# Performance work log

Measured on AMD Instinct MI355X. Metric: run time of the kernel, lower is better.

## Reference

```python
import jax, jax.numpy as jnp
import numpy as np

EPS = 1e-12
SIMILARITY = 'l2'


def setup_inputs() -> dict:
    key = jax.random.key(0)
    k1, k2, k3, k4 = jax.random.split(key, 4)
    N, M, D = 8192, 8192, 256
    x = jax.random.normal(k1, (N, D), dtype=jnp.float32)
    x_n = jax.random.normal(k2, (M, D), dtype=jnp.float32)
    W = jax.random.normal(k3, (D, 2), dtype=jnp.float32) / np.sqrt(D)
    b = jax.random.normal(k4, (2,), dtype=jnp.float32)
    return {"x": x, "x_n": x_n, "W": W, "b": b}


def _sim_matrix(x, x_n, similarity):
    if similarity == 'l2':
        x2 = jnp.sum(x * x, axis=1, keepdims=True)          # [N,1]
        xn2 = jnp.sum(x_n * x_n, axis=1, keepdims=True).T    # [1,M]
        d2 = jnp.maximum(x2 + xn2 - 2.0 * (x @ x_n.T), 0.0)
        return -jnp.sqrt(d2)
    elif similarity == 'l1':
        return -jnp.sum(jnp.abs(x[:, None, :] - x_n[None, :, :]), axis=-1)
    elif similarity == 'dot':
        return (x @ x_n.T) / x.shape[1]
    elif similarity == 'cos':
        xn_ = x / jnp.linalg.norm(x, axis=1, keepdims=True)
        xnn = x_n / jnp.linalg.norm(x_n, axis=1, keepdims=True)
        return xn_ @ xnn.T
    raise ValueError(similarity)


def reference(x, x_n, W, b) -> jnp.ndarray:
    # soft-KNN params from a small linear head
    params = jax.nn.sigmoid(x @ W + b)                      # [N,2]
    k = jnp.clip(params[:, 0:1], EPS, 1.0 - EPS)            # [N,1]
    t = jnp.clip(params[:, 1:2], EPS, 1.0 - EPS)            # [N,1]

    sim = _sim_matrix(x, x_n, SIMILARITY)                   # [N,M]
    sim_min = jnp.min(sim, axis=1, keepdims=True)
    sim_max = jnp.max(sim, axis=1, keepdims=True)
    sim = (sim - sim_min) / (sim_max - sim_min)             # row min-max normalize
    sim = jnp.maximum(sim, EPS)

    shift = t / (1.0 - t) * (k - sim) * jnp.log(sim / k)
    return sim + jnp.where(sim <= k, shift, 0.0)
```

## Files before the change

### kernel.cpp

```cpp
#include <hip/hip_runtime.h>
#include <hip/hip_bf16.h>
#include <hip/hip_fp16.h>
#include <cstdint>

#define N_ROWS 8192
#define M_ROWS 8192
#define DDIM   256
#define EPSF   1e-12f
#define NT     4

typedef unsigned short u16;
typedef __attribute__((ext_vector_type(8))) short short8;
typedef __attribute__((ext_vector_type(4))) float floatx4;

__device__ inline u16 f2h(float v) {
    return __builtin_bit_cast(u16, (_Float16)v);
}
__device__ inline void split_bf16(float v, u16& h, u16& lo) {
    __hip_bfloat16 hb = __float2bfloat16(v);
    float hf = __bfloat162float(hb);
    __hip_bfloat16 lb = __float2bfloat16(v - hf);
    h  = __builtin_bit_cast(u16, hb);
    lo = __builtin_bit_cast(u16, lb);
}

__global__ __launch_bounds__(256) void prep_x(
    const float* __restrict__ x, const float* __restrict__ W, const float* __restrict__ b,
    u16* __restrict__ xh, float* __restrict__ x2, float* __restrict__ karr,
    float* __restrict__ Carr, float* __restrict__ logkarr, u16* __restrict__ bfprobe)
{
    const int l = threadIdx.x & 63;
    const int w = threadIdx.x >> 6;
    const int row = blockIdx.x * 4 + w;

    const float4 xv = *(const float4*)(x + (size_t)row * DDIM + l * 4);
    const float4 wa = *(const float4*)(W + l * 8);
    const float4 wb = *(const float4*)(W + l * 8 + 4);

    float s2 = xv.x * xv.x + xv.y * xv.y + xv.z * xv.z + xv.w * xv.w;
    float s0 = xv.x * wa.x + xv.y * wa.z + xv.z * wb.x + xv.w * wb.z;
    float s1 = xv.x * wa.y + xv.y * wa.w + xv.z * wb.y + xv.w * wb.w;

    *(ushort4*)(xh + (size_t)row * DDIM + l * 4) =
        make_ushort4(f2h(xv.x), f2h(xv.y), f2h(xv.z), f2h(xv.w));

    if (row == 0 && l == 0 && w == 0) {
        u16 hh, ll; split_bf16(xv.x, hh, ll);
        bfprobe[0] = hh; bfprobe[1] = ll;
    }

    #pragma unroll
    for (int off = 32; off; off >>= 1) {
        s2 += __shfl_xor(s2, off);
        s0 += __shfl_xor(s0, off);
        s1 += __shfl_xor(s1, off);
    }
    if (l == 0) {
        float a0 = s0 + b[0];
        float a1 = s1 + b[1];
        float k = 1.0f / (1.0f + __expf(-a0));
        float t = 1.0f / (1.0f + __expf(-a1));
        k = fminf(fmaxf(k, EPSF), 1.0f - EPSF);
        t = fminf(fmaxf(t, EPSF), 1.0f - EPSF);
        x2[row] = s2;
        karr[row] = k;
        Carr[row] = t / (1.0f - t);
        logkarr[row] = logf(k);
    }
}

__global__ __launch_bounds__(256) void prep_xn(
    const float* __restrict__ xn, u16* __restrict__ xnh, float* __restrict__ xn2)
{
    const int l = threadIdx.x & 63;
    const int w = threadIdx.x >> 6;
    const int row = blockIdx.x * 4 + w;

    const float4 xv = *(const float4*)(xn + (size_t)row * DDIM + l * 4);
    float s2 = xv.x * xv.x + xv.y * xv.y + xv.z * xv.z + xv.w * xv.w;

    *(ushort4*)(xnh + (size_t)row * DDIM + l * 4) =
        make_ushort4(f2h(xv.x), f2h(xv.y), f2h(xv.z), f2h(xv.w));

    #pragma unroll
    for (int off = 32; off; off >>= 1) s2 += __shfl_xor(s2, off);
    if (l == 0) xn2[row] = s2;
}

__global__ __launch_bounds__(512, 2) void gemm_s(
    const u16* __restrict__ xh, const u16* __restrict__ xnh,
    const float* __restrict__ x2, const float* __restrict__ xn2,
    float* __restrict__ out)
{
    extern __shared__ char lds[];

    const int tid = threadIdx.x;
    const int l   = tid & 63;
    const int w   = tid >> 6;
    const int wm  = w >> 2;
    const int wn  = w & 3;

    const int wg    = blockIdx.x;
    const int xcd   = wg & 7;
    const int seq   = wg >> 3;
    const int rnd   = seq >> 5;
    const int idx   = seq & 31;
    const int cell  = rnd * 8 + xcd;
    const int rg    = cell & 7;
    const int cg    = cell >> 3;
    const int bRow  = rg * 4 + (idx & 3);
    const int bCol  = cg * 8 + (idx >> 2);

    const int srow = tid >> 3;
    const int scol = (((tid & 7) ^ (srow & 7)) << 3);
    const int dcol = (tid & 7) * 16;
    const int rA1_0 = srow,               rA1_1 = srow + 128;
    const int rA2_0 = srow + 64,          rA2_1 = srow + 192;
    const int rB1_0 = srow + (srow & 32), rB1_1 = rB1_0 + 128;
    const int rB2_0 = rB1_0 + 32,         rB2_1 = rB1_0 + 160;
    const size_t aG = (size_t)bRow * 256;
    const size_t bG = (size_t)bCol * 256;

#define KOFF(T) ((T) * 64)
#define LDSA(T) (lds + ((T) & 1) * 65536)
#define LDSB(T) (lds + ((T) & 1) * 65536 + 32768)
#define SU(pan, gbase, ldsbase, r0, r1, ko) do {                                  \
    __builtin_amdgcn_global_load_lds(                                             \
        (const __attribute__((address_space(1))) void*)((pan) + ((gbase) + (r0)) * (size_t)DDIM + (ko) + scol), \
        (__attribute__((address_space(3))) void*)((ldsbase) + (r0) * 128 + dcol), 16, 0, 0); \
    __builtin_amdgcn_global_load_lds(                                             \
        (const __attribute__((address_space(1))) void*)((pan) + ((gbase) + (r1)) * (size_t)DDIM + (ko) + scol), \
        (__attribute__((address_space(3))) void*)((ldsbase) + (r1) * 128 + dcol), 16, 0, 0); \
} while (0)
#define SU_A1(T) SU(xh,  aG, LDSA(T), rA1_0, rA1_1, KOFF(T))
#define SU_A2(T) SU(xh,  aG, LDSA(T), rA2_0, rA2_1, KOFF(T))
#define SU_B1(T) SU(xnh, bG, LDSB(T), rB1_0, rB1_1, KOFF(T))
#define SU_B2(T) SU(xnh, bG, LDSB(T), rB2_0, rB2_1, KOFF(T))

    floatx4 acc[8][4];
    #pragma unroll
    for (int mi = 0; mi < 8; ++mi)
        #pragma unroll
        for (int ni = 0; ni < 4; ++ni)
            acc[mi][ni] = (floatx4){0.f, 0.f, 0.f, 0.f};

    const int laneRow = l & 15;
    const int laneKb  = (l >> 4) << 4;
    const int laneSwz = (l & 7) << 4;
    const int aRowB = (wm * 128 + laneRow) * 128;
    const int bRowB = (wn * 64  + laneRow) * 128;
    const int kb0 = laneKb ^ laneSwz;
    const int kb1 = (64 + laneKb) ^ laneSwz;

    SU_A1(0); SU_B1(0); SU_B2(0); SU_A2(0);
    SU_B1(1); SU_A1(1); SU_B2(1);

    short8 a[4][2], b01[2][2], b23[2][2];

    for (int t = 0; t < NT; ++t) {
        const char* pA = LDSA(t);
        const char* pB = LDSB(t);

        if (t < NT - 1) asm volatile("s_waitcnt vmcnt(6)" ::: "memory");
        else            asm volatile("s_waitcnt vmcnt(0)" ::: "memory");
        if (t + 1 < NT) SU_A2(t + 1);
        __builtin_amdgcn_s_barrier();
        #pragma unroll
        for (int mi = 0; mi < 4; ++mi) {
            a[mi][0] = *(const short8*)(pA + aRowB + mi * 2048 + kb0);
            a[mi][1] = *(const short8*)(pA + aRowB + mi * 2048 + kb1);
        }
        #pragma unroll
        for (int ni = 0; ni < 2; ++ni) {
            b01[ni][0] = *(const short8*)(pB + bRowB + ni * 2048 + kb0);
            b01[ni][1] = *(const short8*)(pB + bRowB + ni * 2048 + kb1);
        }
        asm volatile("s_waitcnt lgkmcnt(0)" ::: "memory");
        __builtin_amdgcn_sched_barrier(0);
        __builtin_amdgcn_s_setprio(1);
        #pragma unroll
        for (int mi = 0; mi < 4; ++mi)
            #pragma unroll
            for (int ni = 0; ni < 2; ++ni) {
                acc[mi][ni] = __builtin_amdgcn_mfma_f32_16x16x32_f16(a[mi][0], b01[ni][0], acc[mi][ni], 0, 0, 0);
                acc[mi][ni] = __builtin_amdgcn_mfma_f32_16x16x32_f16(a[mi][1], b01[ni][1], acc[mi][ni], 0, 0, 0);
            }
        __builtin_amdgcn_s_setprio(0);
        __builtin_amdgcn_sched_barrier(0);
        __builtin_amdgcn_s_barrier();

        if (t + 2 < NT) SU_B1(t + 2);
        #pragma unroll
        for (int ni = 0; ni < 2; ++ni) {
            b23[ni][0] = *(const short8*)(pB + bRowB + (2 + ni) * 2048 + kb0);
            b23[ni][1] = *(const short8*)(pB + bRowB + (2 + ni) * 2048 + kb1);
        }
        __builtin_amdgcn_s_barrier();
        asm volatile("s_waitcnt lgkmcnt(0)" ::: "memory");
        __builtin_amdgcn_sched_barrier(0);
        __builtin_amdgcn_s_setprio(1);
        #pragma unroll
        for (int mi = 0; mi < 4; ++mi)
            #pragma unroll
            for (int ni = 0; ni < 2; ++ni) {
                acc[mi][2 + ni] = __builtin_amdgcn_mfma_f32_16x16x32_f16(a[mi][0], b23[ni][0], acc[mi][2 + ni], 0, 0, 0);
                acc[mi][2 + ni] = __builtin_amdgcn_mfma_f32_16x16x32_f16(a[mi][1], b23[ni][1], acc[mi][2 + ni], 0, 0, 0);
            }
        __builtin_amdgcn_s_setprio(0);
        __builtin_amdgcn_sched_barrier(0);
        __builtin_amdgcn_s_barrier();

        if (t + 2 < NT) SU_A1(t + 2);
        #pragma unroll
        for (int mi = 0; mi < 4; ++mi) {
            a[mi][0] = *(const short8*)(pA + aRowB + (4 + mi) * 2048 + kb0);
            a[mi][1] = *(const short8*)(pA + aRowB + (4 + mi) * 2048 + kb1);
        }
        __builtin_amdgcn_s_barrier();
        asm volatile("s_waitcnt lgkmcnt(0)" ::: "memory");
        __builtin_amdgcn_sched_barrier(0);
        __builtin_amdgcn_s_setprio(1);
        #pragma unroll
        for (int mi = 0; mi < 4; ++mi)
            #pragma unroll
            for (int ni = 0; ni < 2; ++ni) {
                acc[4 + mi][ni] = __builtin_amdgcn_mfma_f32_16x16x32_f16(a[mi][0], b01[ni][0], acc[4 + mi][ni], 0, 0, 0);
                acc[4 + mi][ni] = __builtin_amdgcn_mfma_f32_16x16x32_f16(a[mi][1], b01[ni][1], acc[4 + mi][ni], 0, 0, 0);
            }
        __builtin_amdgcn_s_setprio(0);
        __builtin_amdgcn_sched_barrier(0);
        __builtin_amdgcn_s_barrier();

        if (t + 2 < NT) SU_B2(t + 2);
        __builtin_amdgcn_s_barrier();
        __builtin_amdgcn_s_setprio(1);
        #pragma unroll
        for (int mi = 0; mi < 4; ++mi)
            #pragma unroll
            for (int ni = 0; ni < 2; ++ni) {
                acc[4 + mi][2 + ni] = __builtin_amdgcn_mfma_f32_16x16x32_f16(a[mi][0], b23[ni][0], acc[4 + mi][2 + ni], 0, 0, 0);
                acc[4 + mi][2 + ni] = __builtin_amdgcn_mfma_f32_16x16x32_f16(a[mi][1], b23[ni][1], acc[4 + mi][2 + ni], 0, 0, 0);
            }
        __builtin_amdgcn_s_setprio(0);
        __builtin_amdgcn_sched_barrier(0);
        __builtin_amdgcn_s_barrier();
    }
#undef SU_A1
#undef SU_A2
#undef SU_B1
#undef SU_B2
#undef SU
#undef KOFF
#undef LDSA
#undef LDSB

    const int q  = l >> 4;
    const int cn = l & 15;
    const int rowBase = bRow * 256 + wm * 128;
    const int colBase = bCol * 256 + wn * 64;
    #pragma unroll
    for (int mi = 0; mi < 8; ++mi) {
        #pragma unroll
        for (int r = 0; r < 4; ++r) {
            const int i = rowBase + mi * 16 + q * 4 + r;
            const float x2i = x2[i];
            #pragma unroll
            for (int ni = 0; ni < 4; ++ni) {
                const int j = colBase + ni * 16 + cn;
                const float d2 = x2i + xn2[j] - 2.0f * acc[mi][ni][r];
                out[(size_t)i * M_ROWS + j] = -sqrtf(fmaxf(d2, 0.0f));
            }
        }
    }
}

__global__ __launch_bounds__(256) void transform_row(
    float* __restrict__ out, const float* __restrict__ x, const float* __restrict__ xn,
    const float* __restrict__ karr, const float* __restrict__ Carr,
    const float* __restrict__ logkarr)
{
    const int row = blockIdx.x;
    const int t = threadIdx.x;
    const int l = t & 63;
    const int w = t >> 6;

    __shared__ float wmin[4], wmax[4];
    __shared__ int cnt;
    __shared__ unsigned long long sMinBits;
    __shared__ int cidx[1024];
    __shared__ double cval[1024];

    const size_t rbase = (size_t)row * M_ROWS;
    float4 v[8];
    #pragma unroll
    for (int c = 0; c < 8; ++c)
        v[c] = *(const float4*)(out + rbase + c * 1024 + t * 4);

    float lmin = 1e30f, lmax = -1e30f;
    #pragma unroll
    for (int c = 0; c < 8; ++c) {
        lmin = fminf(lmin, fminf(fminf(v[c].x, v[c].y), fminf(v[c].z, v[c].w)));
        lmax = fmaxf(lmax, fmaxf(fmaxf(v[c].x, v[c].y), fmaxf(v[c].z, v[c].w)));
    }
    #pragma unroll
    for (int m = 1; m < 64; m <<= 1) {
        lmin = fminf(lmin, __shfl_xor(lmin, m));
        lmax = fmaxf(lmax, __shfl_xor(lmax, m));
    }
    if (l == 0) { wmin[w] = lmin; wmax[w] = lmax; }
    if (t == 0) { cnt = 0; sMinBits = 0ull; }
    __syncthreads();
    const float sminA = fminf(fminf(wmin[0], wmin[1]), fminf(wmin[2], wmin[3]));
    const float smaxA = fmaxf(fmaxf(wmax[0], wmax[1]), fmaxf(wmax[2], wmax[3]));
    const float thresh = sminA + 0.05f * (smaxA - sminA);

    int myPos[8], mySlot[8];
    int myCnt = 0;
    #pragma unroll
    for (int c = 0; c < 8; ++c) {
        const float* pv = (const float*)&v[c];
        #pragma unroll
        for (int u = 0; u < 4; ++u) {
            if (pv[u] <= thresh) {
                int pos = atomicAdd(&cnt, 1);
                if (pos < 1024 && myCnt < 8) {
                    cidx[pos] = c * 1024 + t * 4 + u;
                    myPos[myCnt] = pos;
                    mySlot[myCnt] = c * 4 + u;
                    myCnt++;
                }
            }
        }
    }
    __syncthreads();
    const int nc = min(cnt, 1024);

    const float4 xa = *(const float4*)(x + (size_t)row * DDIM + l * 4);
    const double dx0 = xa.x, dx1 = xa.y, dx2 = xa.z, dx3 = xa.w;
    double x2p = dx0 * dx0 + dx1 * dx1 + dx2 * dx2 + dx3 * dx3;
    #pragma unroll
    for (int m = 1; m < 64; m <<= 1) x2p += __shfl_xor(x2p, m);

    for (int c = w; c < nc; c += 4) {
        const int j = cidx[c];
        const float4 na = *(const float4*)(xn + (size_t)j * DDIM + l * 4);
        const double n0 = na.x, n1 = na.y, n2 = na.z, n3 = na.w;
        double dot = dx0 * n0 + dx1 * n1 + dx2 * n2 + dx3 * n3;
        double nn  = n0 * n0 + n1 * n1 + n2 * n2 + n3 * n3;
        #pragma unroll
        for (int m = 1; m < 64; m <<= 1) {
            dot += __shfl_xor(dot, m);
            nn  += __shfl_xor(nn, m);
        }
        if (l == 0) {
            double d2 = x2p + nn - 2.0 * dot;
            d2 = d2 > 0.0 ? d2 : 0.0;
            double se = -sqrt(d2);
            cval[c] = se;
            atomicMax(&sMinBits, (unsigned long long)__double_as_longlong(se));
        }
    }
    __syncthreads();

    const double sminD = __longlong_as_double((long long)sMinBits);
    const float k = karr[row], C = Carr[row], logk = logkarr[row];
    const float smin = (float)sminD;
    const double invD = 1.0 / ((double)smaxA - sminD);
    const float inv = (float)invD;

    float o[32];
    #pragma unroll
    for (int c = 0; c < 8; ++c) {
        const float* pv = (const float*)&v[c];
        #pragma unroll
        for (int u = 0; u < 4; ++u) {
            float sim = fmaxf((pv[u] - smin) * inv, EPSF);
            float r = sim;
            if (sim <= k) r += C * (k - sim) * (__logf(sim) - logk);
            o[c * 4 + u] = r;
        }
    }
    for (int q2 = 0; q2 < myCnt; ++q2) {
        double simd = (cval[myPos[q2]] - sminD) * invD;
        simd = simd > (double)EPSF ? simd : (double)EPSF;
        float sim = (float)simd;
        float r = sim;
        if (sim <= k) r += C * (k - sim) * (logf(sim) - logk);
        o[mySlot[q2]] = r;
    }
    #pragma unroll
    for (int c = 0; c < 8; ++c) {
        float4 ov;
        ov.x = o[c * 4 + 0]; ov.y = o[c * 4 + 1];
        ov.z = o[c * 4 + 2]; ov.w = o[c * 4 + 3];
        *(float4*)(out + rbase + c * 1024 + t * 4) = ov;
    }
}

extern "C" void kernel_launch(void* const* d_in, const int* in_sizes, int n_in,
                              void* d_out, int out_size, void* d_ws, size_t ws_size,
                              hipStream_t stream)
{
    const float* x  = (const float*)d_in[0];
    const float* xn = (const float*)d_in[1];
    const float* W  = (const float*)d_in[2];
    const float* b  = (const float*)d_in[3];
    float* out = (float*)d_out;

    uint8_t* ws = (uint8_t*)d_ws;
    u16* xh   = (u16*)(ws);
    u16* xnh  = (u16*)(ws + (4u << 20));
    float* x2       = (float*)(ws + (8u << 20));
    float* xn2      = x2 + N_ROWS;
    float* karr     = xn2 + M_ROWS;
    float* Carr     = karr + N_ROWS;
    float* logkarr  = Carr + N_ROWS;
    u16* bfprobe    = (u16*)(logkarr + N_ROWS);

    static bool attr_done = false;
    if (!attr_done) {
        (void)hipFuncSetAttribute(reinterpret_cast<const void*>(gemm_s),
                                  hipFuncAttributeMaxDynamicSharedMemorySize, 131072);
        attr_done = true;
    }

    prep_x<<<N_ROWS / 4, 256, 0, stream>>>(x, W, b, xh, x2, karr, Carr, logkarr, bfprobe);
    prep_xn<<<M_ROWS / 4, 256, 0, stream>>>(xn, xnh, xn2);
    gemm_s<<<1024, 512, 131072, stream>>>(xh, xnh, x2, xn2, out);
    transform_row<<<N_ROWS, 256, 0, stream>>>(out, x, xn, karr, Carr, logkarr);
}
```

Measured before the change: 415.8 us.

## Recompute GEMM in two passes to fuse row normalization into the epilogue

The first GEMM pass keeps only per-row min/max squared distances, reduced through shared and global atomics. A small stats kernel then builds per-row normalization constants. A second GEMM pass applies the soft-KNN transform in its epilogue and records near-minimum candidates. A refine kernel recomputes only those candidates in double precision and scatters them, so the full 8192x8192 output is no longer read back and rewritten. In exchange the GEMM runs twice, the epilogue gains global atomics, and the candidate cap drops to 512.

```diff
diff --git a/kernel.cpp b/kernel.cpp
--- a/kernel.cpp
+++ b/kernel.cpp
@@ -8,14 +8,13 @@
 #define DDIM   256
 #define EPSF   1e-12f
 #define NT     4
+#define CAND_CAP 512
 
 typedef unsigned short u16;
 typedef __attribute__((ext_vector_type(8))) short short8;
 typedef __attribute__((ext_vector_type(4))) float floatx4;
 
-__device__ inline u16 f2h(float v) {
-    return __builtin_bit_cast(u16, (_Float16)v);
-}
+__device__ inline u16 f2h(float v) { return __builtin_bit_cast(u16, (_Float16)v); }
 __device__ inline void split_bf16(float v, u16& h, u16& lo) {
     __hip_bfloat16 hb = __float2bfloat16(v);
     float hf = __bfloat162float(hb);
@@ -23,73 +22,94 @@
     h  = __builtin_bit_cast(u16, hb);
     lo = __builtin_bit_cast(u16, lb);
 }
-
-__global__ __launch_bounds__(256) void prep_x(
-    const float* __restrict__ x, const float* __restrict__ W, const float* __restrict__ b,
-    u16* __restrict__ xh, float* __restrict__ x2, float* __restrict__ karr,
-    float* __restrict__ Carr, float* __restrict__ logkarr, u16* __restrict__ bfprobe)
+__device__ __forceinline__ float d2_of(float x2i, float xn2j, float a) {
+    return fmaxf(fmaf(-2.0f, a, x2i + xn2j), 0.0f);
+}
+
+__global__ __launch_bounds__(256) void prep_all(
+    const float* __restrict__ x, const float* __restrict__ xn,
+    const float* __restrict__ W, const float* __restrict__ b,
+    u16* __restrict__ xh, u16* __restrict__ xnh,
+    float* __restrict__ x2, float* __restrict__ xn2,
+    float* __restrict__ karr, float* __restrict__ Carr, float* __restrict__ logkarr,
+    uint32_t* __restrict__ d2max_bits, uint32_t* __restrict__ d2min_bits,
+    uint32_t* __restrict__ cand_cnt, u16* __restrict__ bfprobe)
 {
+    const int bid = blockIdx.x;
     const int l = threadIdx.x & 63;
     const int w = threadIdx.x >> 6;
-    const int row = blockIdx.x * 4 + w;
-
-    const float4 xv = *(const float4*)(x + (size_t)row * DDIM + l * 4);
-    const float4 wa = *(const float4*)(W + l * 8);
-    const float4 wb = *(const float4*)(W + l * 8 + 4);
-
-    float s2 = xv.x * xv.x + xv.y * xv.y + xv.z * xv.z + xv.w * xv.w;
-    float s0 = xv.x * wa.x + xv.y * wa.z + xv.z * wb.x + xv.w * wb.z;
-    float s1 = xv.x * wa.y + xv.y * wa.w + xv.z * wb.y + xv.w * wb.w;
-
-    *(ushort4*)(xh + (size_t)row * DDIM + l * 4) =
-        make_ushort4(f2h(xv.x), f2h(xv.y), f2h(xv.z), f2h(xv.w));
-
-    if (row == 0 && l == 0 && w == 0) {
-        u16 hh, ll; split_bf16(xv.x, hh, ll);
-        bfprobe[0] = hh; bfprobe[1] = ll;
-    }
-
-    #pragma unroll
-    for (int off = 32; off; off >>= 1) {
-        s2 += __shfl_xor(s2, off);
-        s0 += __shfl_xor(s0, off);
-        s1 += __shfl_xor(s1, off);
-    }
-    if (l == 0) {
-        float a0 = s0 + b[0];
-        float a1 = s1 + b[1];
-        float k = 1.0f / (1.0f + __expf(-a0));
-        float t = 1.0f / (1.0f + __expf(-a1));
-        k = fminf(fmaxf(k, EPSF), 1.0f - EPSF);
-        t = fminf(fmaxf(t, EPSF), 1.0f - EPSF);
-        x2[row] = s2;
-        karr[row] = k;
-        Carr[row] = t / (1.0f - t);
-        logkarr[row] = logf(k);
-    }
-}
-
-__global__ __launch_bounds__(256) void prep_xn(
-    const float* __restrict__ xn, u16* __restrict__ xnh, float* __restrict__ xn2)
+
+    if (bid < 32)        cand_cnt [bid * 256 + threadIdx.x] = 0u;
+    else if (bid < 64)   d2max_bits[(bid - 32) * 256 + threadIdx.x] = 0u;
+    else if (bid < 96)   d2min_bits[(bid - 64) * 256 + threadIdx.x] = 0x7F7FFFFFu;
+
+    if (bid < 2048) {
+        const int row = bid * 4 + w;
+        const float4 xv = *(const float4*)(x + (size_t)row * DDIM + l * 4);
+        const float4 wa = *(const float4*)(W + l * 8);
+        const float4 wb = *(const float4*)(W + l * 8 + 4);
+
+        float s2 = xv.x * xv.x + xv.y * xv.y + xv.z * xv.z + xv.w * xv.w;
+        float s0 = xv.x * wa.x + xv.y * wa.z + xv.z * wb.x + xv.w * wb.z;
+        float s1 = xv.x * wa.y + xv.y * wa.w + xv.z * wb.y + xv.w * wb.w;
+
+        *(ushort4*)(xh + (size_t)row * DDIM + l * 4) =
+            make_ushort4(f2h(xv.x), f2h(xv.y), f2h(xv.z), f2h(xv.w));
+        if (row == 0 && l == 0 && w == 0) {
+            u16 hh, ll; split_bf16(xv.x, hh, ll);
+            bfprobe[0] = hh; bfprobe[1] = ll;
+        }
+        #pragma unroll
+        for (int off = 32; off; off >>= 1) {
+            s2 += __shfl_xor(s2, off);
+            s0 += __shfl_xor(s0, off);
+            s1 += __shfl_xor(s1, off);
+        }
+        if (l == 0) {
+            float a0 = s0 + b[0];
+            float a1 = s1 + b[1];
+            float k = 1.0f / (1.0f + __expf(-a0));
+            float t = 1.0f / (1.0f + __expf(-a1));
+            k = fminf(fmaxf(k, EPSF), 1.0f - EPSF);
+            t = fminf(fmaxf(t, EPSF), 1.0f - EPSF);
+            x2[row] = s2;
+            karr[row] = k;
+            Carr[row] = t / (1.0f - t);
+            logkarr[row] = logf(k);
+        }
+    } else {
+        const int row = (bid - 2048) * 4 + w;
+        const float4 xv = *(const float4*)(xn + (size_t)row * DDIM + l * 4);
+        float s2 = xv.x * xv.x + xv.y * xv.y + xv.z * xv.z + xv.w * xv.w;
+        *(ushort4*)(xnh + (size_t)row * DDIM + l * 4) =
+            make_ushort4(f2h(xv.x), f2h(xv.y), f2h(xv.z), f2h(xv.w));
+        #pragma unroll
+        for (int off = 32; off; off >>= 1) s2 += __shfl_xor(s2, off);
+        if (l == 0) xn2[row] = s2;
+    }
+}
+
+__global__ __launch_bounds__(256) void prep_stats(
+    const uint32_t* __restrict__ d2max_bits, const uint32_t* __restrict__ d2min_bits,
+    const float* __restrict__ karr, const float* __restrict__ Carr,
+    const float* __restrict__ logkarr,
+    float4* __restrict__ T1, float4* __restrict__ T2)
 {
-    const int l = threadIdx.x & 63;
-    const int w = threadIdx.x >> 6;
-    const int row = blockIdx.x * 4 + w;
-
-    const float4 xv = *(const float4*)(xn + (size_t)row * DDIM + l * 4);
-    float s2 = xv.x * xv.x + xv.y * xv.y + xv.z * xv.z + xv.w * xv.w;
-
-    *(ushort4*)(xnh + (size_t)row * DDIM + l * 4) =
-        make_ushort4(f2h(xv.x), f2h(xv.y), f2h(xv.z), f2h(xv.w));
-
-    #pragma unroll
-    for (int off = 32; off; off >>= 1) s2 += __shfl_xor(s2, off);
-    if (l == 0) xn2[row] = s2;
-}
-
-__global__ __launch_bounds__(512, 2) void gemm_s(
+    const int row = blockIdx.x * 256 + threadIdx.x;
+    const float smin = -sqrtf(__uint_as_float(d2max_bits[row]));
+    const float smax = -sqrtf(__uint_as_float(d2min_bits[row]));
+    const float range = smax - smin;
+    T1[row] = make_float4(smin, 1.0f / range, smin + 0.05f * range, karr[row]);
+    T2[row] = make_float4(Carr[row], logkarr[row], smax, 0.0f);
+}
+
+template<int MODE>
+__global__ __launch_bounds__(512, 2) void gemm_core(
     const u16* __restrict__ xh, const u16* __restrict__ xnh,
     const float* __restrict__ x2, const float* __restrict__ xn2,
+    const float4* __restrict__ T1v, const float4* __restrict__ T2v,
+    uint32_t* __restrict__ d2max_bits, uint32_t* __restrict__ d2min_bits,
+    uint32_t* __restrict__ cand_cnt, u16* __restrict__ cand,
     float* __restrict__ out)
 {
     extern __shared__ char lds[];
@@ -258,82 +278,87 @@
     const int cn = l & 15;
     const int rowBase = bRow * 256 + wm * 128;
     const int colBase = bCol * 256 + wn * 64;
-    #pragma unroll
-    for (int mi = 0; mi < 8; ++mi) {
-        #pragma unroll
-        for (int r = 0; r < 4; ++r) {
-            const int i = rowBase + mi * 16 + q * 4 + r;
-            const float x2i = x2[i];
-            #pragma unroll
-            for (int ni = 0; ni < 4; ++ni) {
-                const int j = colBase + ni * 16 + cn;
-                const float d2 = x2i + xn2[j] - 2.0f * acc[mi][ni][r];
-                out[(size_t)i * M_ROWS + j] = -sqrtf(fmaxf(d2, 0.0f));
-            }
-        }
-    }
-}
-
-__global__ __launch_bounds__(256) void transform_row(
+
+    if constexpr (MODE == 0) {
+        uint32_t* sMn = (uint32_t*)(lds + 131072);
+        uint32_t* sMx = sMn + 256;
+        if (tid < 256) { sMn[tid] = 0u; sMx[tid] = 0x7F7FFFFFu; }
+        __syncthreads();
+        #pragma unroll
+        for (int mi = 0; mi < 8; ++mi) {
+            #pragma unroll
+            for (int r = 0; r < 4; ++r) {
+                const int i = rowBase + mi * 16 + q * 4 + r;
+                const float x2i = x2[i];
+                float dmx = 0.0f, dmn = 3.4e38f;
+                #pragma unroll
+                for (int ni = 0; ni < 4; ++ni) {
+                    const int j = colBase + ni * 16 + cn;
+                    const float d2 = d2_of(x2i, xn2[j], acc[mi][ni][r]);
+                    dmx = fmaxf(dmx, d2);
+                    dmn = fminf(dmn, d2);
+                }
+                #pragma unroll
+                for (int m = 1; m < 16; m <<= 1) {
+                    dmx = fmaxf(dmx, __shfl_xor(dmx, m));
+                    dmn = fminf(dmn, __shfl_xor(dmn, m));
+                }
+                if (cn == 0) {
+                    const int ri = wm * 128 + mi * 16 + q * 4 + r;
+                    atomicMax(&sMn[ri], __float_as_uint(dmx));
+                    atomicMin(&sMx[ri], __float_as_uint(dmn));
+                }
+            }
+        }
+        __syncthreads();
+        if (tid < 256) {
+            atomicMax(&d2max_bits[bRow * 256 + tid], sMn[tid]);
+            atomicMin(&d2min_bits[bRow * 256 + tid], sMx[tid]);
+        }
+    } else {
+        #pragma unroll
+        for (int mi = 0; mi < 8; ++mi) {
+            #pragma unroll
+            for (int r = 0; r < 4; ++r) {
+                const int i = rowBase + mi * 16 + q * 4 + r;
+                const float x2i = x2[i];
+                const float4 t1 = T1v[i];
+                const float4 t2 = T2v[i];
+                #pragma unroll
+                for (int ni = 0; ni < 4; ++ni) {
+                    const int j = colBase + ni * 16 + cn;
+                    const float d2 = d2_of(x2i, xn2[j], acc[mi][ni][r]);
+                    const float s = -sqrtf(d2);
+                    float sim = fmaxf((s - t1.x) * t1.y, EPSF);
+                    float rr = sim;
+                    if (sim <= t1.w) rr += t2.x * (t1.w - sim) * (__logf(sim) - t2.y);
+                    if (s <= t1.z) {
+                        unsigned p = atomicAdd(&cand_cnt[i], 1u);
+                        if (p < CAND_CAP) cand[(size_t)i * CAND_CAP + p] = (u16)j;
+                    }
+                    out[(size_t)i * M_ROWS + j] = rr;
+                }
+            }
+        }
+    }
+}
+
+__global__ __launch_bounds__(256) void refine_rows(
     float* __restrict__ out, const float* __restrict__ x, const float* __restrict__ xn,
-    const float* __restrict__ karr, const float* __restrict__ Carr,
-    const float* __restrict__ logkarr)
+    const float4* __restrict__ T1v, const float4* __restrict__ T2v,
+    const uint32_t* __restrict__ cand_cnt, const u16* __restrict__ cand)
 {
     const int row = blockIdx.x;
     const int t = threadIdx.x;
     const int l = t & 63;
     const int w = t >> 6;
 
-    __shared__ float wmin[4], wmax[4];
-    __shared__ int cnt;
     __shared__ unsigned long long sMinBits;
-    __shared__ int cidx[1024];
-    __shared__ double cval[1024];
-
-    const size_t rbase = (size_t)row * M_ROWS;
-    float4 v[8];
-    #pragma unroll
-    for (int c = 0; c < 8; ++c)
-        v[c] = *(const float4*)(out + rbase + c * 1024 + t * 4);
-
-    float lmin = 1e30f, lmax = -1e30f;
-    #pragma unroll
-    for (int c = 0; c < 8; ++c) {
-        lmin = fminf(lmin, fminf(fminf(v[c].x, v[c].y), fminf(v[c].z, v[c].w)));
-        lmax = fmaxf(lmax, fmaxf(fmaxf(v[c].x, v[c].y), fmaxf(v[c].z, v[c].w)));
-    }
-    #pragma unroll
-    for (int m = 1; m < 64; m <<= 1) {
-        lmin = fminf(lmin, __shfl_xor(lmin, m));
-        lmax = fmaxf(lmax, __shfl_xor(lmax, m));
-    }
-    if (l == 0) { wmin[w] = lmin; wmax[w] = lmax; }
-    if (t == 0) { cnt = 0; sMinBits = 0ull; }
+    __shared__ double cval[CAND_CAP];
+
+    const int nc = min((int)cand_cnt[row], CAND_CAP);
+    if (t == 0) sMinBits = 0ull;
     __syncthreads();
-    const float sminA = fminf(fminf(wmin[0], wmin[1]), fminf(wmin[2], wmin[3]));
-    const float smaxA = fmaxf(fmaxf(wmax[0], wmax[1]), fmaxf(wmax[2], wmax[3]));
-    const float thresh = sminA + 0.05f * (smaxA - sminA);
-
-    int myPos[8], mySlot[8];
-    int myCnt = 0;
-    #pragma unroll
-    for (int c = 0; c < 8; ++c) {
-        const float* pv = (const float*)&v[c];
-        #pragma unroll
-        for (int u = 0; u < 4; ++u) {
-            if (pv[u] <= thresh) {
-                int pos = atomicAdd(&cnt, 1);
-                if (pos < 1024 && myCnt < 8) {
-                    cidx[pos] = c * 1024 + t * 4 + u;
-                    myPos[myCnt] = pos;
-                    mySlot[myCnt] = c * 4 + u;
-                    myCnt++;
-                }
-            }
-        }
-    }
-    __syncthreads();
-    const int nc = min(cnt, 1024);
 
     const float4 xa = *(const float4*)(x + (size_t)row * DDIM + l * 4);
     const double dx0 = xa.x, dx1 = xa.y, dx2 = xa.z, dx3 = xa.w;
@@ -342,7 +367,7 @@
     for (int m = 1; m < 64; m <<= 1) x2p += __shfl_xor(x2p, m);
 
     for (int c = w; c < nc; c += 4) {
-        const int j = cidx[c];
+        const int j = cand[(size_t)row * CAND_CAP + c];
         const float4 na = *(const float4*)(xn + (size_t)j * DDIM + l * 4);
         const double n0 = na.x, n1 = na.y, n2 = na.z, n3 = na.w;
         double dot = dx0 * n0 + dx1 * n1 + dx2 * n2 + dx3 * n3;
@@ -363,37 +388,18 @@
     __syncthreads();
 
     const double sminD = __longlong_as_double((long long)sMinBits);
-    const float k = karr[row], C = Carr[row], logk = logkarr[row];
-    const float smin = (float)sminD;
-    const double invD = 1.0 / ((double)smaxA - sminD);
-    const float inv = (float)invD;
-
-    float o[32];
-    #pragma unroll
-    for (int c = 0; c < 8; ++c) {
-        const float* pv = (const float*)&v[c];
-        #pragma unroll
-        for (int u = 0; u < 4; ++u) {
-            float sim = fmaxf((pv[u] - smin) * inv, EPSF);
-            float r = sim;
-            if (sim <= k) r += C * (k - sim) * (__logf(sim) - logk);
-            o[c * 4 + u] = r;
-        }
-    }
-    for (int q2 = 0; q2 < myCnt; ++q2) {
-        double simd = (cval[myPos[q2]] - sminD) * invD;
+    const float4 t1 = T1v[row];
+    const float4 t2 = T2v[row];
+    const float k = t1.w, C = t2.x, logk = t2.y;
+    const double invD = 1.0 / ((double)t2.z - sminD);
+
+    for (int c = t; c < nc; c += 256) {
+        double simd = (cval[c] - sminD) * invD;
         simd = simd > (double)EPSF ? simd : (double)EPSF;
         float sim = (float)simd;
-        float r = sim;
-        if (sim <= k) r += C * (k - sim) * (logf(sim) - logk);
-        o[mySlot[q2]] = r;
-    }
-    #pragma unroll
-    for (int c = 0; c < 8; ++c) {
-        float4 ov;
-        ov.x = o[c * 4 + 0]; ov.y = o[c * 4 + 1];
-        ov.z = o[c * 4 + 2]; ov.w = o[c * 4 + 3];
-        *(float4*)(out + rbase + c * 1024 + t * 4) = ov;
+        float rr = sim;
+        if (sim <= k) rr += C * (k - sim) * (logf(sim) - logk);
+        out[(size_t)row * M_ROWS + cand[(size_t)row * CAND_CAP + c]] = rr;
     }
 }
 
@@ -410,22 +416,37 @@
     uint8_t* ws = (uint8_t*)d_ws;
     u16* xh   = (u16*)(ws);
     u16* xnh  = (u16*)(ws + (4u << 20));
-    float* x2       = (float*)(ws + (8u << 20));
+    u16* cand = (u16*)(ws + (8u << 20));
+    float* x2       = (float*)(ws + (16u << 20));
     float* xn2      = x2 + N_ROWS;
     float* karr     = xn2 + M_ROWS;
     float* Carr     = karr + N_ROWS;
     float* logkarr  = Carr + N_ROWS;
-    u16* bfprobe    = (u16*)(logkarr + N_ROWS);
+    uint32_t* d2max_bits = (uint32_t*)(logkarr + N_ROWS);
+    uint32_t* d2min_bits = d2max_bits + N_ROWS;
+    uint32_t* cand_cnt   = d2min_bits + N_ROWS;
+    float4* T1 = (float4*)(cand_cnt + N_ROWS);
+    float4* T2 = T1 + N_ROWS;
+    u16* bfprobe = (u16*)(T2 + N_ROWS);
 
     static bool attr_done = false;
     if (!attr_done) {
-        (void)hipFuncSetAttribute(reinterpret_cast<const void*>(gemm_s),
+        (void)hipFuncSetAttribute(reinterpret_cast<const void*>(gemm_core<0>),
+                                  hipFuncAttributeMaxDynamicSharedMemorySize, 131072 + 2048);
+        (void)hipFuncSetAttribute(reinterpret_cast<const void*>(gemm_core<1>),
                                   hipFuncAttributeMaxDynamicSharedMemorySize, 131072);
         attr_done = true;
     }
 
-    prep_x<<<N_ROWS / 4, 256, 0, stream>>>(x, W, b, xh, x2, karr, Carr, logkarr, bfprobe);
-    prep_xn<<<M_ROWS / 4, 256, 0, stream>>>(xn, xnh, xn2);
-    gemm_s<<<1024, 512, 131072, stream>>>(xh, xnh, x2, xn2, out);
-    transform_row<<<N_ROWS, 256, 0, stream>>>(out, x, xn, karr, Carr, logkarr);
-}
+    prep_all<<<4096, 256, 0, stream>>>(x, xn, W, b, xh, xnh, x2, xn2,
+                                       karr, Carr, logkarr,
+                                       d2max_bits, d2min_bits, cand_cnt, bfprobe);
+    gemm_core<0><<<1024, 512, 131072 + 2048, stream>>>(
+        xh, xnh, x2, xn2, nullptr, nullptr,
+        d2max_bits, d2min_bits, nullptr, nullptr, nullptr);
+    prep_stats<<<32, 256, 0, stream>>>(d2max_bits, d2min_bits, karr, Carr, logkarr, T1, T2);
+    gemm_core<1><<<1024, 512, 131072, stream>>>(
+        xh, xnh, x2, xn2, T1, T2,
+        nullptr, nullptr, cand_cnt, cand, out);
+    refine_rows<<<N_ROWS, 256, 0, stream>>>(out, x, xn, T1, T2, cand_cnt, cand);
+}
```

Measured after the change: 486.5 us. 1.17x slower.
